# Kernel tuning notes

Hardware: AMD Instinct MI355X
Metric: run time of the kernel (lower is better)

The kernel has to match this reference:

```python
import math
import jax, jax.numpy as jnp
import numpy as np

B, L, D, H = 2, 2048, 1024, 16
DT = D // H  # 64


def setup_inputs() -> dict:
    key = jax.random.key(0)
    ks = jax.random.split(key, 11)
    s = 1.0 / math.sqrt(D)
    return {
        "q": jax.random.normal(ks[0], (B, L, D), jnp.float32),
        "k": jax.random.normal(ks[1], (B, L, D), jnp.float32),
        "v": jax.random.normal(ks[2], (B, L, D), jnp.float32),
        "Wq": jax.random.normal(ks[3], (D, D), jnp.float32) * s,
        "bq": jnp.zeros((D,), jnp.float32),
        "Wk": jax.random.normal(ks[4], (D, D), jnp.float32) * s,
        "bk": jnp.zeros((D,), jnp.float32),
        "Wv": jax.random.normal(ks[5], (D, D), jnp.float32) * s,
        "bv": jnp.zeros((D,), jnp.float32),
        "Wc": jax.random.normal(ks[6], (D, D), jnp.float32) * s,
        "bc": jnp.zeros((D,), jnp.float32),
    }


def reference(q, k, v, Wq, bq, Wk, bk, Wv, bv, Wc, bc):
    # Linear projections (torch Linear: x @ W^T + b)
    Q = q @ Wq.T + bq
    K = k @ Wk.T + bk
    V = v @ Wv.T + bv
    # split(): plain view/reshape [B, L, D] -> [B, H, L, d] (faithful to source)
    Qs = Q.reshape(B, H, L, DT)
    Ks = K.reshape(B, H, L, DT)
    Vs = V.reshape(B, H, L, DT)
    # k_t is also a plain reshape [B,H,L,d] -> [B,H,d,L] (NOT a transpose)
    Kt = Ks.reshape(B, H, DT, L)
    score = jnp.matmul(Qs, Kt) / math.sqrt(DT)  # [B, H, L, L]
    # nn.Softmax() with no dim on 4D tensor -> legacy dim=1 (head axis)
    attn = jax.nn.softmax(score, axis=1)
    out = jnp.matmul(attn, Vs)  # [B, H, L, d]
    out = out.reshape(B, L, D)  # concat() is also a plain reshape
    return out @ Wc.T + bc
```

## Files before the change

### kernel.cpp

```cpp
#include <hip/hip_runtime.h>
#include <hip/hip_bf16.h>


using u16   = unsigned short;
using f16   = _Float16;
using f16x2 = _Float16 __attribute__((ext_vector_type(2)));
using f16x8 = _Float16 __attribute__((ext_vector_type(8)));
using bf16x8 = __bf16 __attribute__((ext_vector_type(8)));
using f32x4  = float  __attribute__((ext_vector_type(4)));

__device__ __forceinline__ u16 f2bf(float f) {
    __bf16 h = (__bf16)f;
    return __builtin_bit_cast(u16, h);
}
__device__ __forceinline__ float ex2(float x) {
    return __builtin_amdgcn_exp2f(x);
}
__device__ __forceinline__ bf16x8 ldfrag(const u16* p) {
    bf16x8 r; __builtin_memcpy(&r, p, 16); return r;
}
__device__ __forceinline__ f16x8 ldfrag16(const u16* p) {
    f16x8 r; __builtin_memcpy(&r, p, 16); return r;
}
__device__ __forceinline__ unsigned pkrtz(float a, float b) {
    return __builtin_bit_cast(unsigned, __builtin_amdgcn_cvt_pkrtz(a, b));
}
__device__ __forceinline__ f16x2 u2h(unsigned u) { return __builtin_bit_cast(f16x2, u); }
__device__ __forceinline__ unsigned h2u(f16x2 h) { return __builtin_bit_cast(unsigned, h); }

__device__ __forceinline__ void stage16(const float* p, u16* d) {
    #pragma unroll
    for (int u = 0; u < 16; u += 4) {
        float4 t = *reinterpret_cast<const float4*>(p + u);
        d[u + 0] = f2bf(t.x); d[u + 1] = f2bf(t.y);
        d[u + 2] = f2bf(t.z); d[u + 3] = f2bf(t.w);
    }
}
__device__ __forceinline__ void stage16(const u16* p, u16* d) {
    #pragma unroll
    for (int u = 0; u < 16; u += 8)
        *reinterpret_cast<uint4*>(d + u) = *reinterpret_cast<const uint4*>(p + u);
}

template <typename XT, typename WT, typename OT, bool F16O>
__device__ __forceinline__ void gemm_body(
    const XT* __restrict__ X,
    const WT* __restrict__ W, const float* __restrict__ bias,
    OT* __restrict__ C, float scale,
    u16 (*lX)[72], u16 (*lW)[72])
{
    const int tid  = threadIdx.x;
    const int lane = tid & 63;
    const int wv   = tid >> 6;
    const int wm   = (wv >> 2) * 64;
    const int wn   = (wv & 3) * 32;
    const int m0 = blockIdx.x * 128;
    const int n0 = blockIdx.y * 128;
    const int sr = tid >> 2;
    const int sq = (tid & 3) * 16;
    const int fm = lane & 15;
    const int g  = lane >> 4;
    const int fk = g * 8;

    f32x4 acc[4][2] = {};

    for (int k0 = 0; k0 < 1024; k0 += 64) {
        stage16(X + (size_t)(m0 + sr) * 1024 + k0 + sq, &lX[sr][sq]);
        stage16(W + (size_t)(n0 + sr) * 1024 + k0 + sq, &lW[sr][sq]);
        __syncthreads();
        #pragma unroll
        for (int kb = 0; kb < 2; ++kb) {
            bf16x8 a[4], bb[2];
            #pragma unroll
            for (int mb = 0; mb < 4; ++mb)
                a[mb] = ldfrag(&lX[wm + mb * 16 + fm][kb * 32 + fk]);
            #pragma unroll
            for (int nb = 0; nb < 2; ++nb)
                bb[nb] = ldfrag(&lW[wn + nb * 16 + fm][kb * 32 + fk]);
            #pragma unroll
            for (int mb = 0; mb < 4; ++mb)
                #pragma unroll
                for (int nb = 0; nb < 2; ++nb)
                    acc[mb][nb] = __builtin_amdgcn_mfma_f32_16x16x32_bf16(
                        a[mb], bb[nb], acc[mb][nb], 0, 0, 0);
        }
        __syncthreads();
    }

    #pragma unroll
    for (int mb = 0; mb < 4; ++mb) {
        #pragma unroll
        for (int nb = 0; nb < 2; ++nb) {
            const int row = m0 + wm + mb * 16 + g * 4;
            const int col = n0 + wn + nb * 16 + fm;
            const float bv = bias[col];
            #pragma unroll
            for (int r = 0; r < 4; ++r) {
                const float val = (acc[mb][nb][r] + bv) * scale;
                OT* p = C + (size_t)(row + r) * 1024 + col;
                if constexpr (F16O) {
                    f16 h = (f16)val;
                    *p = __builtin_bit_cast(u16, h);
                } else if constexpr (__is_same(OT, u16)) {
                    *p = f2bf(val);
                } else {
                    *p = val;
                }
            }
        }
    }
}

template <typename T>
__global__ __launch_bounds__(512) void gemm_qkv_t(
    const T* __restrict__ q, const T* __restrict__ k,
    const T* __restrict__ v,
    const T* __restrict__ Wq, const float* __restrict__ bq,
    const T* __restrict__ Wk, const float* __restrict__ bk,
    const T* __restrict__ Wv, const float* __restrict__ bv,
    u16* __restrict__ Q16, u16* __restrict__ K16, u16* __restrict__ V16,
    float qscale)
{
    __shared__ u16 lX[128][72];
    __shared__ u16 lW[128][72];
    const int z = blockIdx.z;
    const T* X = (z == 0) ? q  : (z == 1) ? k  : v;
    const T* W = (z == 0) ? Wq : (z == 1) ? Wk : Wv;
    const float* B = (z == 0) ? bq : (z == 1) ? bk : bv;
    u16*         C = (z == 0) ? Q16 : (z == 1) ? K16 : V16;
    const float  s = (z == 0) ? qscale : 1.0f;
    gemm_body<T, T, u16, true>(X, W, B, C, s, lX, lW);
}

template <typename WT>
__global__ __launch_bounds__(512) void gemm_final_t(
    const u16* __restrict__ X,
    const WT* __restrict__ W, const float* __restrict__ bias,
    float* __restrict__ C)
{
    __shared__ u16 lX[128][72];
    __shared__ u16 lW[128][72];
    gemm_body<u16, WT, float, false>(X, W, bias, C, 1.0f, lX, lW);
}

__global__ __launch_bounds__(256) void prep_bf16(
    const float* __restrict__ q, const float* __restrict__ k,
    const float* __restrict__ v,
    const float* __restrict__ Wq, const float* __restrict__ Wk,
    const float* __restrict__ Wv, const float* __restrict__ Wc,
    u16* __restrict__ qb, u16* __restrict__ kb, u16* __restrict__ vb,
    u16* __restrict__ wqb, u16* __restrict__ wkb,
    u16* __restrict__ wvb, u16* __restrict__ wcb)
{
    const long long NC = 2097152;
    for (long long c = (long long)blockIdx.x * 256 + threadIdx.x; c < NC;
         c += (long long)gridDim.x * 256) {
        const float* src; u16* dst; long long off;
        if (c < 1572864) {
            if (c < 524288)       { src = q; dst = qb; off = c; }
            else if (c < 1048576) { src = k; dst = kb; off = c - 524288; }
            else                  { src = v; dst = vb; off = c - 1048576; }
        } else {
            const long long wI = c - 1572864;
            if (wI < 131072)      { src = Wq; dst = wqb; off = wI; }
            else if (wI < 262144) { src = Wk; dst = wkb; off = wI - 131072; }
            else if (wI < 393216) { src = Wv; dst = wvb; off = wI - 262144; }
            else                  { src = Wc; dst = wcb; off = wI - 393216; }
        }
        const float* p = src + off * 8;
        const float4 a  = reinterpret_cast<const float4*>(p)[0];
        const float4 b2 = reinterpret_cast<const float4*>(p)[1];
        u16 d[8];
        d[0] = f2bf(a.x);  d[1] = f2bf(a.y);  d[2] = f2bf(a.z);  d[3] = f2bf(a.w);
        d[4] = f2bf(b2.x); d[5] = f2bf(b2.y); d[6] = f2bf(b2.z); d[7] = f2bf(b2.w);
        *reinterpret_cast<uint4*>(dst + off * 8) = *reinterpret_cast<uint4*>(d);
    }
}

template <int NS>
__global__ __launch_bounds__(256) void presum_o(
    const u16* __restrict__ a, const u16* __restrict__ b,
    const u16* __restrict__ c, const u16* __restrict__ d,
    u16* __restrict__ o)
{
    const long long NC = 524288;
    for (long long i = (long long)blockIdx.x * 256 + threadIdx.x; i < NC;
         i += (long long)gridDim.x * 256) {
        const long long e0 = i * 8;
        const bf16x8 va = ldfrag(a + e0);
        const bf16x8 vb = ldfrag(b + e0);
        bf16x8 vc, vd;
        if constexpr (NS >= 3) vc = ldfrag(c + e0);
        if constexpr (NS >= 4) vd = ldfrag(d + e0);
        u16 r[8];
        #pragma unroll
        for (int e = 0; e < 8; ++e) {
            float s = (float)va[e] + (float)vb[e];
            if constexpr (NS >= 3) s += (float)vc[e];
            if constexpr (NS >= 4) s += (float)vd[e];
            r[e] = f2bf(s);
        }
        *reinterpret_cast<uint4*>(o + e0) = *reinterpret_cast<uint4*>(r);
    }
}

__global__ __launch_bounds__(256) void tp_kv2(
    const u16* __restrict__ kin, u16* __restrict__ kout,
    const u16* __restrict__ vin, u16* __restrict__ vout)
{
    __shared__ u16 t[64][80];
    const int which = (blockIdx.x >> 10) & 1;
    const int bx    = blockIdx.x & 1023;
    const u16* in_  = which ? vin  : kin;
    u16*       out_ = which ? vout : kout;
    const int tid = threadIdx.x;
    const int bh  = bx >> 5;
    const int tt  = bx & 31;
    const size_t base = (size_t)bh * 131072;
    const int C         = which ? 64 : 2048;
    const int r0        = which ? tt * 64 : 0;
    const int c0        = which ? 0 : tt * 64;
    const int outstride = which ? 2048 : 64;
    const u16* in = in_ + base;
    u16* out      = out_ + base;

    #pragma unroll
    for (int half = 0; half < 2; ++half) {
        const int rr = (tid >> 3) + half * 32;
        const int cb = tid & 7;
        const int cbs = cb ^ ((rr >> 3) & 7);
        *reinterpret_cast<uint4*>(&t[rr][cbs * 8]) =
            *reinterpret_cast<const uint4*>(in + (size_t)(r0 + rr) * C + c0 + cb * 8);
    }
    __syncthreads();
    #pragma unroll
    for (int half = 0; half < 2; ++half) {
        const int c  = (tid >> 3) + half * 32;
        const int rb = tid & 7;
        u16 vv[8];
        #pragma unroll
        for (int e = 0; e < 8; ++e) {
            const int r = rb * 8 + e;
            const int cbs2 = (c >> 3) ^ ((r >> 3) & 7);
            vv[e] = t[r][cbs2 * 8 + (c & 7)];
        }
        *reinterpret_cast<uint4*>(out + (size_t)(c0 + c) * outstride + r0 + rb * 8) =
            *reinterpret_cast<uint4*>(vv);
    }
}

__global__ __launch_bounds__(1024) void attn_fused(
    const u16* __restrict__ Qb, const u16* __restrict__ KT,
    const u16* __restrict__ VT, u16* __restrict__ O0,
    u16* __restrict__ O1, u16* __restrict__ O2, u16* __restrict__ O3,
    int jsplit)
{
    __shared__ unsigned expS[16][64][20];
    __shared__ unsigned rcpS[64][20];

    const int tid  = threadIdx.x;
    const int w    = tid >> 6;
    const int lane = tid & 63;
    const int fm   = lane & 15;
    const int g    = lane >> 4;
    const int fk   = g * 8;
    const int g4   = g * 4;
    const int g2   = g * 2;

    int b, it, js;
    u16* Ob;
    if (jsplit == 4) {
        const int grp = blockIdx.x & 7;
        b  = grp >> 2;
        js = grp & 3;
        it = blockIdx.x >> 3;
        Ob = (js == 0) ? O0 : (js == 1) ? O1 : (js == 2) ? O2 : O3;
    } else if (jsplit == 2) {
        const int grp = blockIdx.x & 3;
        b  = grp >> 1;
        js = grp & 1;
        it = blockIdx.x >> 2;
        Ob = js ? O1 : O0;
    } else {
        b  = blockIdx.x >> 5;
        it = blockIdx.x & 31;
        js = 0;
        Ob = O0;
    }
    const int jlen  = 2048 / jsplit;
    const int jbase = js * jlen;
    const int i0    = it * 64;
    const size_t hb = ((size_t)b * 2048 + (size_t)w * 128) * 1024;

    f16x8 qa[4][2];
    #pragma unroll
    for (int m = 0; m < 4; ++m)
        #pragma unroll
        for (int kb = 0; kb < 2; ++kb)
            qa[m][kb] = ldfrag16(Qb + hb + (size_t)(i0 + m * 16 + fm) * 64 + kb * 32 + fk);

    f32x4 oacc[4][4] = {};

    const int nt  = jlen >> 5;

    auto qk_tile = [&](int j0) {
        f16x8 kf[2][2];
        #pragma unroll
        for (int kb = 0; kb < 2; ++kb)
            #pragma unroll
            for (int nb = 0; nb < 2; ++nb)
                kf[kb][nb] = ldfrag16(KT + hb + (size_t)(j0 + nb * 16 + fm) * 64
                                               + kb * 32 + fk);
        #pragma unroll
        for (int m = 0; m < 4; ++m) {
            f32x4 st[2] = {};
            #pragma unroll
            for (int kb = 0; kb < 2; ++kb)
                #pragma unroll
                for (int nb = 0; nb < 2; ++nb)
                    st[nb] = __builtin_amdgcn_mfma_f32_16x16x32_f16(
                        kf[kb][nb], qa[m][kb], st[nb], 0, 0, 0);
            const int row = m * 16 + fm;
            #pragma unroll
            for (int nb = 0; nb < 2; ++nb) {
                uint2 ew2;
                ew2.x = pkrtz(ex2(st[nb][0]), ex2(st[nb][1]));
                ew2.y = pkrtz(ex2(st[nb][2]), ex2(st[nb][3]));
                *reinterpret_cast<uint2*>(&expS[w][row][nb * 8 + g2]) = ew2;
            }
        }
    };

    qk_tile(jbase);

    for (int t = 0; t < nt; ++t) {
        const int j0 = jbase + (t << 5);
        __syncthreads();
        f16x8 vf[4];
        #pragma unroll
        for (int nb = 0; nb < 4; ++nb)
            vf[nb] = ldfrag16(VT + hb + (size_t)(nb * 16 + fm) * 2048 + j0 + fk);
        {
            const int i  = tid >> 4;
            const int jp = tid & 15;
            unsigned eh[16];
            #pragma unroll
            for (int h = 0; h < 16; ++h) eh[h] = expS[h][i][jp];
            const f16x2 s0 = (u2h(eh[0])  + u2h(eh[1]))  + (u2h(eh[2])  + u2h(eh[3]));
            const f16x2 s1 = (u2h(eh[4])  + u2h(eh[5]))  + (u2h(eh[6])  + u2h(eh[7]));
            const f16x2 s2 = (u2h(eh[8])  + u2h(eh[9]))  + (u2h(eh[10]) + u2h(eh[11]));
            const f16x2 s3 = (u2h(eh[12]) + u2h(eh[13])) + (u2h(eh[14]) + u2h(eh[15]));
            const f16x2 ts = (s0 + s1) + (s2 + s3);
            rcpS[i][jp] = pkrtz(__builtin_amdgcn_rcpf((float)ts[0]),
                                __builtin_amdgcn_rcpf((float)ts[1]));
        }
        __syncthreads();
        #pragma unroll
        for (int m = 0; m < 4; ++m) {
            const int row = m * 16 + fm;
            const uint4 ew = *reinterpret_cast<const uint4*>(&expS[w][row][g4]);
            const uint4 rw = *reinterpret_cast<const uint4*>(&rcpS[row][g4]);
            uint4 pw;
            pw.x = h2u(u2h(ew.x) * u2h(rw.x));
            pw.y = h2u(u2h(ew.y) * u2h(rw.y));
            pw.z = h2u(u2h(ew.z) * u2h(rw.z));
            pw.w = h2u(u2h(ew.w) * u2h(rw.w));
            const f16x8 pa = __builtin_bit_cast(f16x8, pw);
            #pragma unroll
            for (int nb = 0; nb < 4; ++nb)
                oacc[m][nb] = __builtin_amdgcn_mfma_f32_16x16x32_f16(
                    pa, vf[nb], oacc[m][nb], 0, 0, 0);
        }
        if (t + 1 < nt) qk_tile(j0 + 32);
    }

    #pragma unroll
    for (int m = 0; m < 4; ++m)
        #pragma unroll
        for (int nb = 0; nb < 4; ++nb)
            #pragma unroll
            for (int r = 0; r < 4; ++r) {
                const int i = i0 + m * 16 + g4 + r;
                Ob[hb + (size_t)i * 64 + nb * 16 + fm] = f2bf(oacc[m][nb][r]);
            }
}

extern "C" void kernel_launch(void* const* d_in, const int* in_sizes, int n_in,
                              void* d_out, int out_size, void* d_ws, size_t ws_size,
                              hipStream_t stream)
{
    const float* q  = (const float*)d_in[0];
    const float* k  = (const float*)d_in[1];
    const float* v  = (const float*)d_in[2];
    const float* Wq = (const float*)d_in[3];
    const float* bq = (const float*)d_in[4];
    const float* Wk = (const float*)d_in[5];
    const float* bk = (const float*)d_in[6];
    const float* Wv = (const float*)d_in[7];
    const float* bv = (const float*)d_in[8];
    const float* Wc = (const float*)d_in[9];
    const float* bc = (const float*)d_in[10];
    float* out = (float*)d_out;

    const size_t MD = (size_t)4096 * 1024;
    const size_t WM = MD / 4;
    u16* W0 = (u16*)d_ws;
    u16* W1 = W0 + MD;
    u16* W2 = W1 + MD;
    u16* W3 = W2 + MD;
    u16* W4 = W3 + MD;
    u16* W5 = W4 + MD;
    u16* W6 = W5 + MD;
    u16* qb  = W6 + MD;
    u16* kb  = qb + MD;
    u16* vb  = kb + MD;
    u16* wqb = vb + MD;
    u16* wkb = wqb + WM;
    u16* wvb = wkb + WM;
    u16* wcb = wvb + WM;

    int jsplit = 1;
    if      (ws_size >= 7 * MD * sizeof(u16)) jsplit = 4;
    else if (ws_size >= 5 * MD * sizeof(u16)) jsplit = 2;
    const bool prep = ws_size >= 11 * MD * sizeof(u16);

    const float qscale = 0.125f * 1.4426950408889634f;

    if (prep)
        prep_bf16<<<dim3(2048), dim3(256), 0, stream>>>(
            q, k, v, Wq, Wk, Wv, Wc, qb, kb, vb, wqb, wkb, wvb, wcb);

    if (prep)
        gemm_qkv_t<u16><<<dim3(32, 8, 3), dim3(512), 0, stream>>>(
            qb, kb, vb, wqb, bq, wkb, bk, wvb, bv, W0, W1, W2, qscale);
    else
        gemm_qkv_t<float><<<dim3(32, 8, 3), dim3(512), 0, stream>>>(
            q, k, v, Wq, bq, Wk, bk, Wv, bv, W0, W1, W2, qscale);

    tp_kv2<<<dim3(2048), dim3(256), 0, stream>>>(W1, W3, W2, W4);

    const int agrid = (jsplit == 4) ? 256 : (jsplit == 2) ? 128 : 64;
    attn_fused<<<dim3(agrid), dim3(1024), 0, stream>>>(
        W0, W3, W4, W1, W2, W5, W6, jsplit);

    const u16* Xf = W1;
    if (jsplit == 4) {
        presum_o<4><<<dim3(2048), dim3(256), 0, stream>>>(W1, W2, W5, W6, W0);
        Xf = W0;
    } else if (jsplit == 2) {
        presum_o<2><<<dim3(2048), dim3(256), 0, stream>>>(W1, W2, nullptr, nullptr, W0);
        Xf = W0;
    }

    if (prep)
        gemm_final_t<u16><<<dim3(32, 8), dim3(512), 0, stream>>>(Xf, wcb, bc, out);
    else
        gemm_final_t<float><<<dim3(32, 8), dim3(512), 0, stream>>>(Xf, Wc, bc, out);
}
```

Measured before the change: 184.2 us.

## Retile fused attention to 512-thread blocks handling two heads per wave

Each attention block now covers 32 query rows instead of 64 and uses 512 threads. Each wave processes two heads rather than one. The grid doubles, the shared exp and reciprocal buffers halve, and launch bounds request four blocks per CU, all aimed at higher occupancy and cheaper block-wide barriers. In exchange, each K and V fragment load is reused across only 32 query rows, so K/V traffic from L2 per unit of work doubles.

```diff
diff --git a/kernel.cpp b/kernel.cpp
--- a/kernel.cpp
+++ b/kernel.cpp
@@ -249,17 +249,18 @@
     }
 }
 
-__global__ __launch_bounds__(1024) void attn_fused(
+__global__ __launch_bounds__(512, 4) void attn_fused(
     const u16* __restrict__ Qb, const u16* __restrict__ KT,
     const u16* __restrict__ VT, u16* __restrict__ O0,
     u16* __restrict__ O1, u16* __restrict__ O2, u16* __restrict__ O3,
     int jsplit)
 {
-    __shared__ unsigned expS[16][64][20];
-    __shared__ unsigned rcpS[64][20];
+    __shared__ unsigned expS[16][32][20];
+    __shared__ unsigned rcpS[32][20];
 
     const int tid  = threadIdx.x;
-    const int w    = tid >> 6;
+    const int wv   = tid >> 6;
+    const int h0   = wv * 2;
     const int lane = tid & 63;
     const int fm   = lane & 15;
     const int g    = lane >> 4;
@@ -282,51 +283,59 @@
         it = blockIdx.x >> 2;
         Ob = js ? O1 : O0;
     } else {
-        b  = blockIdx.x >> 5;
-        it = blockIdx.x & 31;
+        b  = blockIdx.x & 1;
+        it = blockIdx.x >> 1;
         js = 0;
         Ob = O0;
     }
     const int jlen  = 2048 / jsplit;
     const int jbase = js * jlen;
-    const int i0    = it * 64;
-    const size_t hb = ((size_t)b * 2048 + (size_t)w * 128) * 1024;
-
-    f16x8 qa[4][2];
-    #pragma unroll
-    for (int m = 0; m < 4; ++m)
-        #pragma unroll
-        for (int kb = 0; kb < 2; ++kb)
-            qa[m][kb] = ldfrag16(Qb + hb + (size_t)(i0 + m * 16 + fm) * 64 + kb * 32 + fk);
-
-    f32x4 oacc[4][4] = {};
+    const int i0    = it * 32;
+    size_t hb[2];
+    hb[0] = ((size_t)b * 2048 + (size_t)h0 * 128) * 1024;
+    hb[1] = hb[0] + 131072;
+
+    f16x8 qa[2][2][2];
+    #pragma unroll
+    for (int hh = 0; hh < 2; ++hh)
+        #pragma unroll
+        for (int m = 0; m < 2; ++m)
+            #pragma unroll
+            for (int kb = 0; kb < 2; ++kb)
+                qa[hh][m][kb] = ldfrag16(Qb + hb[hh]
+                    + (size_t)(i0 + m * 16 + fm) * 64 + kb * 32 + fk);
+
+    f32x4 oacc[2][2][4] = {};
 
     const int nt  = jlen >> 5;
 
     auto qk_tile = [&](int j0) {
-        f16x8 kf[2][2];
-        #pragma unroll
-        for (int kb = 0; kb < 2; ++kb)
-            #pragma unroll
-            for (int nb = 0; nb < 2; ++nb)
-                kf[kb][nb] = ldfrag16(KT + hb + (size_t)(j0 + nb * 16 + fm) * 64
-                                               + kb * 32 + fk);
-        #pragma unroll
-        for (int m = 0; m < 4; ++m) {
-            f32x4 st[2] = {};
+        #pragma unroll
+        for (int hh = 0; hh < 2; ++hh) {
+            f16x8 kf[2][2];
             #pragma unroll
             for (int kb = 0; kb < 2; ++kb)
                 #pragma unroll
                 for (int nb = 0; nb < 2; ++nb)
-                    st[nb] = __builtin_amdgcn_mfma_f32_16x16x32_f16(
-                        kf[kb][nb], qa[m][kb], st[nb], 0, 0, 0);
-            const int row = m * 16 + fm;
-            #pragma unroll
-            for (int nb = 0; nb < 2; ++nb) {
-                uint2 ew2;
-                ew2.x = pkrtz(ex2(st[nb][0]), ex2(st[nb][1]));
-                ew2.y = pkrtz(ex2(st[nb][2]), ex2(st[nb][3]));
-                *reinterpret_cast<uint2*>(&expS[w][row][nb * 8 + g2]) = ew2;
+                    kf[kb][nb] = ldfrag16(KT + hb[hh]
+                        + (size_t)(j0 + nb * 16 + fm) * 64 + kb * 32 + fk);
+            #pragma unroll
+            for (int m = 0; m < 2; ++m) {
+                f32x4 st[2] = {};
+                #pragma unroll
+                for (int kb = 0; kb < 2; ++kb)
+                    #pragma unroll
+                    for (int nb = 0; nb < 2; ++nb)
+                        st[nb] = __builtin_amdgcn_mfma_f32_16x16x32_f16(
+                            kf[kb][nb], qa[hh][m][kb], st[nb], 0, 0, 0);
+                const int row = m * 16 + fm;
+                #pragma unroll
+                for (int nb = 0; nb < 2; ++nb) {
+                    uint2 ew2;
+                    ew2.x = pkrtz(ex2(st[nb][0]), ex2(st[nb][1]));
+                    ew2.y = pkrtz(ex2(st[nb][2]), ex2(st[nb][3]));
+                    *reinterpret_cast<uint2*>(&expS[h0 + hh][row][nb * 8 + g2]) = ew2;
+                }
             }
         }
     };
@@ -336,10 +345,6 @@
     for (int t = 0; t < nt; ++t) {
         const int j0 = jbase + (t << 5);
         __syncthreads();
-        f16x8 vf[4];
-        #pragma unroll
-        for (int nb = 0; nb < 4; ++nb)
-            vf[nb] = ldfrag16(VT + hb + (size_t)(nb * 16 + fm) * 2048 + j0 + fk);
         {
             const int i  = tid >> 4;
             const int jp = tid & 15;
@@ -356,33 +361,44 @@
         }
         __syncthreads();
         #pragma unroll
-        for (int m = 0; m < 4; ++m) {
-            const int row = m * 16 + fm;
-            const uint4 ew = *reinterpret_cast<const uint4*>(&expS[w][row][g4]);
-            const uint4 rw = *reinterpret_cast<const uint4*>(&rcpS[row][g4]);
-            uint4 pw;
-            pw.x = h2u(u2h(ew.x) * u2h(rw.x));
-            pw.y = h2u(u2h(ew.y) * u2h(rw.y));
-            pw.z = h2u(u2h(ew.z) * u2h(rw.z));
-            pw.w = h2u(u2h(ew.w) * u2h(rw.w));
-            const f16x8 pa = __builtin_bit_cast(f16x8, pw);
+        for (int hh = 0; hh < 2; ++hh) {
+            f16x8 vf[4];
             #pragma unroll
             for (int nb = 0; nb < 4; ++nb)
-                oacc[m][nb] = __builtin_amdgcn_mfma_f32_16x16x32_f16(
-                    pa, vf[nb], oacc[m][nb], 0, 0, 0);
+                vf[nb] = ldfrag16(VT + hb[hh]
+                    + (size_t)(nb * 16 + fm) * 2048 + j0 + fk);
+            #pragma unroll
+            for (int m = 0; m < 2; ++m) {
+                const int row = m * 16 + fm;
+                const uint4 ew = *reinterpret_cast<const uint4*>(&expS[h0 + hh][row][g4]);
+                const uint4 rw = *reinterpret_cast<const uint4*>(&rcpS[row][g4]);
+                uint4 pw;
+                pw.x = h2u(u2h(ew.x) * u2h(rw.x));
+                pw.y = h2u(u2h(ew.y) * u2h(rw.y));
+                pw.z = h2u(u2h(ew.z) * u2h(rw.z));
+                pw.w = h2u(u2h(ew.w) * u2h(rw.w));
+                const f16x8 pa = __builtin_bit_cast(f16x8, pw);
+                #pragma unroll
+                for (int nb = 0; nb < 4; ++nb)
+                    oacc[hh][m][nb] = __builtin_amdgcn_mfma_f32_16x16x32_f16(
+                        pa, vf[nb], oacc[hh][m][nb], 0, 0, 0);
+            }
         }
         if (t + 1 < nt) qk_tile(j0 + 32);
     }
 
     #pragma unroll
-    for (int m = 0; m < 4; ++m)
-        #pragma unroll
-        for (int nb = 0; nb < 4; ++nb)
-            #pragma unroll
-            for (int r = 0; r < 4; ++r) {
-                const int i = i0 + m * 16 + g4 + r;
-                Ob[hb + (size_t)i * 64 + nb * 16 + fm] = f2bf(oacc[m][nb][r]);
-            }
+    for (int hh = 0; hh < 2; ++hh)
+        #pragma unroll
+        for (int m = 0; m < 2; ++m)
+            #pragma unroll
+            for (int nb = 0; nb < 4; ++nb)
+                #pragma unroll
+                for (int r = 0; r < 4; ++r) {
+                    const int i = i0 + m * 16 + g4 + r;
+                    Ob[hb[hh] + (size_t)i * 64 + nb * 16 + fm] =
+                        f2bf(oacc[hh][m][nb][r]);
+                }
 }
 
 extern "C" void kernel_launch(void* const* d_in, const int* in_sizes, int n_in,
@@ -439,8 +455,8 @@
 
     tp_kv2<<<dim3(2048), dim3(256), 0, stream>>>(W1, W3, W2, W4);
 
-    const int agrid = (jsplit == 4) ? 256 : (jsplit == 2) ? 128 : 64;
-    attn_fused<<<dim3(agrid), dim3(1024), 0, stream>>>(
+    const int agrid = (jsplit == 4) ? 512 : (jsplit == 2) ? 256 : 128;
+    attn_fused<<<dim3(agrid), dim3(512), 0, stream>>>(
         W0, W3, W4, W1, W2, W5, W6, jsplit);
 
     const u16* Xf = W1;
```

Measured after the change: 257.2 us. 39.6% more time.

## Process 64-column tiles per barrier pair with XOR-swizzled shared exp buffers

Applied to the files above, without the earlier changes.

Doubles the key-column tile handled per iteration of the head-axis softmax attention loop from 32 to 64, so each pair of block-wide barriers covers twice as much work. This halves the number of __syncthreads calls. The shared exp and reciprocal buffers are widened to 32 columns and indexed with an XOR swizzle to avoid LDS bank conflicts, since the old padding-based layout no longer applies. It uses more shared memory and more live work per stage, which may reduce latency hiding.

```diff
diff --git a/kernel.cpp b/kernel.cpp
--- a/kernel.cpp
+++ b/kernel.cpp
@@ -255,8 +255,8 @@
     u16* __restrict__ O1, u16* __restrict__ O2, u16* __restrict__ O3,
     int jsplit)
 {
-    __shared__ unsigned expS[16][64][20];
-    __shared__ unsigned rcpS[64][20];
+    __shared__ unsigned expS[16][64][32];
+    __shared__ unsigned rcpS[64][32];
 
     const int tid  = threadIdx.x;
     const int w    = tid >> 6;
@@ -292,6 +292,8 @@
     const int i0    = it * 64;
     const size_t hb = ((size_t)b * 2048 + (size_t)w * 128) * 1024;
 
+    auto fx = [](int r) { return ((r >> 1) & 3) << 2; };
+
     f16x8 qa[4][2];
     #pragma unroll
     for (int m = 0; m < 4; ++m)
@@ -301,9 +303,9 @@
 
     f32x4 oacc[4][4] = {};
 
-    const int nt  = jlen >> 5;
-
-    auto qk_tile = [&](int j0) {
+    const int nt = jlen >> 6;
+
+    auto qk_half = [&](int j0, int cb) {
         f16x8 kf[2][2];
         #pragma unroll
         for (int kb = 0; kb < 2; ++kb)
@@ -321,45 +323,28 @@
                     st[nb] = __builtin_amdgcn_mfma_f32_16x16x32_f16(
                         kf[kb][nb], qa[m][kb], st[nb], 0, 0, 0);
             const int row = m * 16 + fm;
+            const int fr  = fx(row);
             #pragma unroll
             for (int nb = 0; nb < 2; ++nb) {
                 uint2 ew2;
                 ew2.x = pkrtz(ex2(st[nb][0]), ex2(st[nb][1]));
                 ew2.y = pkrtz(ex2(st[nb][2]), ex2(st[nb][3]));
-                *reinterpret_cast<uint2*>(&expS[w][row][nb * 8 + g2]) = ew2;
+                *reinterpret_cast<uint2*>(&expS[w][row][(cb + nb * 8 + g2) ^ fr]) = ew2;
             }
         }
     };
 
-    qk_tile(jbase);
-
-    for (int t = 0; t < nt; ++t) {
-        const int j0 = jbase + (t << 5);
-        __syncthreads();
+    auto pv_half = [&](int jh, int cb) {
         f16x8 vf[4];
         #pragma unroll
         for (int nb = 0; nb < 4; ++nb)
-            vf[nb] = ldfrag16(VT + hb + (size_t)(nb * 16 + fm) * 2048 + j0 + fk);
-        {
-            const int i  = tid >> 4;
-            const int jp = tid & 15;
-            unsigned eh[16];
-            #pragma unroll
-            for (int h = 0; h < 16; ++h) eh[h] = expS[h][i][jp];
-            const f16x2 s0 = (u2h(eh[0])  + u2h(eh[1]))  + (u2h(eh[2])  + u2h(eh[3]));
-            const f16x2 s1 = (u2h(eh[4])  + u2h(eh[5]))  + (u2h(eh[6])  + u2h(eh[7]));
-            const f16x2 s2 = (u2h(eh[8])  + u2h(eh[9]))  + (u2h(eh[10]) + u2h(eh[11]));
-            const f16x2 s3 = (u2h(eh[12]) + u2h(eh[13])) + (u2h(eh[14]) + u2h(eh[15]));
-            const f16x2 ts = (s0 + s1) + (s2 + s3);
-            rcpS[i][jp] = pkrtz(__builtin_amdgcn_rcpf((float)ts[0]),
-                                __builtin_amdgcn_rcpf((float)ts[1]));
-        }
-        __syncthreads();
+            vf[nb] = ldfrag16(VT + hb + (size_t)(nb * 16 + fm) * 2048 + jh + fk);
         #pragma unroll
         for (int m = 0; m < 4; ++m) {
             const int row = m * 16 + fm;
-            const uint4 ew = *reinterpret_cast<const uint4*>(&expS[w][row][g4]);
-            const uint4 rw = *reinterpret_cast<const uint4*>(&rcpS[row][g4]);
+            const int fr  = fx(row);
+            const uint4 ew = *reinterpret_cast<const uint4*>(&expS[w][row][(cb + g4) ^ fr]);
+            const uint4 rw = *reinterpret_cast<const uint4*>(&rcpS[row][(cb + g4) ^ fr]);
             uint4 pw;
             pw.x = h2u(u2h(ew.x) * u2h(rw.x));
             pw.y = h2u(u2h(ew.y) * u2h(rw.y));
@@ -371,7 +356,41 @@
                 oacc[m][nb] = __builtin_amdgcn_mfma_f32_16x16x32_f16(
                     pa, vf[nb], oacc[m][nb], 0, 0, 0);
         }
-        if (t + 1 < nt) qk_tile(j0 + 32);
+    };
+
+    auto sum_half = [&](int i, int p) {
+        unsigned eh[16];
+        #pragma unroll
+        for (int h = 0; h < 16; ++h) eh[h] = expS[h][i][p];
+        const f16x2 s0 = (u2h(eh[0])  + u2h(eh[1]))  + (u2h(eh[2])  + u2h(eh[3]));
+        const f16x2 s1 = (u2h(eh[4])  + u2h(eh[5]))  + (u2h(eh[6])  + u2h(eh[7]));
+        const f16x2 s2 = (u2h(eh[8])  + u2h(eh[9]))  + (u2h(eh[10]) + u2h(eh[11]));
+        const f16x2 s3 = (u2h(eh[12]) + u2h(eh[13])) + (u2h(eh[14]) + u2h(eh[15]));
+        const f16x2 ts = (s0 + s1) + (s2 + s3);
+        rcpS[i][p] = pkrtz(__builtin_amdgcn_rcpf((float)ts[0]),
+                           __builtin_amdgcn_rcpf((float)ts[1]));
+    };
+
+    qk_half(jbase, 0);
+    qk_half(jbase + 32, 16);
+
+    for (int t = 0; t < nt; ++t) {
+        const int j0 = jbase + (t << 6);
+        __syncthreads();
+        {
+            const int i = tid >> 4;
+            const int p = (tid & 15) ^ fx(i);
+            sum_half(i, p);
+            __builtin_amdgcn_sched_barrier(0);
+            sum_half(i, p + 16);
+        }
+        __syncthreads();
+        pv_half(j0, 0);
+        pv_half(j0 + 32, 16);
+        if (t + 1 < nt) {
+            qk_half(j0 + 64, 0);
+            qk_half(j0 + 96, 16);
+        }
     }
 
     #pragma unroll
```

Measured after the change: 231.3 us. 1.26x slower.

## Fuse K transpose into K projection GEMM epilogue via LDS staging

Applied to the files above, without the earlier changes.

The K projection moves into its own GEMM kernel whose epilogue stages the tile in shared memory and writes it directly in the transposed per-head layout the attention kernel expects. This removes the K half of the separate transpose kernel, cutting one global write and read of K. The QKV GEMM becomes a Q/V-only launch and the transpose kernel now handles only V. This adds an extra kernel launch and a less coalesced transposed store path. The float-input variant stages via stage16, which looks type-dependent and may not handle float inputs correctly.

```diff
diff --git a/kernel.cpp b/kernel.cpp
--- a/kernel.cpp
+++ b/kernel.cpp
@@ -112,24 +112,102 @@
 }
 
 template <typename T>
-__global__ __launch_bounds__(512) void gemm_qkv_t(
-    const T* __restrict__ q, const T* __restrict__ k,
-    const T* __restrict__ v,
+__global__ __launch_bounds__(512) void gemm_qv_t(
+    const T* __restrict__ q, const T* __restrict__ v,
     const T* __restrict__ Wq, const float* __restrict__ bq,
-    const T* __restrict__ Wk, const float* __restrict__ bk,
     const T* __restrict__ Wv, const float* __restrict__ bv,
-    u16* __restrict__ Q16, u16* __restrict__ K16, u16* __restrict__ V16,
-    float qscale)
+    u16* __restrict__ Q16, u16* __restrict__ V16, float qscale)
 {
     __shared__ u16 lX[128][72];
     __shared__ u16 lW[128][72];
     const int z = blockIdx.z;
-    const T* X = (z == 0) ? q  : (z == 1) ? k  : v;
-    const T* W = (z == 0) ? Wq : (z == 1) ? Wk : Wv;
-    const float* B = (z == 0) ? bq : (z == 1) ? bk : bv;
-    u16*         C = (z == 0) ? Q16 : (z == 1) ? K16 : V16;
-    const float  s = (z == 0) ? qscale : 1.0f;
+    const T* X = z ? v  : q;
+    const T* W = z ? Wv : Wq;
+    const float* B = z ? bv : bq;
+    u16*         C = z ? V16 : Q16;
+    const float  s = z ? 1.0f : qscale;
     gemm_body<T, T, u16, true>(X, W, B, C, s, lX, lW);
+}
+
+template <typename T>
+__global__ __launch_bounds__(512) void gemm_kt_t(
+    const T* __restrict__ X, const T* __restrict__ W,
+    const float* __restrict__ bias, u16* __restrict__ KT)
+{
+    __shared__ u16 lbuf[2][128][72];
+    u16 (*lX)[72] = lbuf[0];
+    u16 (*lW)[72] = lbuf[1];
+
+    const int tid  = threadIdx.x;
+    const int lane = tid & 63;
+    const int wv   = tid >> 6;
+    const int wm   = (wv >> 2) * 64;
+    const int wn   = (wv & 3) * 32;
+    const int m0 = blockIdx.x * 128;
+    const int n0 = blockIdx.y * 128;
+    const int sr = tid >> 2;
+    const int sq = (tid & 3) * 16;
+    const int fm = lane & 15;
+    const int g  = lane >> 4;
+    const int fk = g * 8;
+
+    f32x4 acc[4][2] = {};
+
+    for (int k0 = 0; k0 < 1024; k0 += 64) {
+        stage16(X + (size_t)(m0 + sr) * 1024 + k0 + sq, &lX[sr][sq]);
+        stage16(W + (size_t)(n0 + sr) * 1024 + k0 + sq, &lW[sr][sq]);
+        __syncthreads();
+        #pragma unroll
+        for (int kb = 0; kb < 2; ++kb) {
+            bf16x8 a[4], bb[2];
+            #pragma unroll
+            for (int mb = 0; mb < 4; ++mb)
+                a[mb] = ldfrag(&lX[wm + mb * 16 + fm][kb * 32 + fk]);
+            #pragma unroll
+            for (int nb = 0; nb < 2; ++nb)
+                bb[nb] = ldfrag(&lW[wn + nb * 16 + fm][kb * 32 + fk]);
+            #pragma unroll
+            for (int mb = 0; mb < 4; ++mb)
+                #pragma unroll
+                for (int nb = 0; nb < 2; ++nb)
+                    acc[mb][nb] = __builtin_amdgcn_mfma_f32_16x16x32_bf16(
+                        a[mb], bb[nb], acc[mb][nb], 0, 0, 0);
+        }
+        __syncthreads();
+    }
+
+    u16 (*T2)[136] = reinterpret_cast<u16 (*)[136]>(&lbuf[0][0][0]);
+    #pragma unroll
+    for (int mb = 0; mb < 4; ++mb)
+        #pragma unroll
+        for (int nb = 0; nb < 2; ++nb) {
+            const int colL = wn + nb * 16 + fm;
+            const float bv = bias[n0 + colL];
+            #pragma unroll
+            for (int r = 0; r < 4; ++r) {
+                const int row = wm + mb * 16 + g * 4 + r;
+                const f16 hv = (f16)(acc[mb][nb][r] + bv);
+                T2[row][colL] = __builtin_bit_cast(u16, hv);
+            }
+        }
+    __syncthreads();
+
+    const int bb2 = m0 >> 11;
+    const int hh  = (m0 >> 7) & 15;
+    u16* slab = KT + (size_t)bb2 * 2097152 + (size_t)hh * 131072;
+    const int kr   = tid >> 1;
+    const int half = tid & 1;
+    const int hi   = kr >> 7;
+    const int jloc = kr & 127;
+    u16 buf[32];
+    #pragma unroll
+    for (int e = 0; e < 32; ++e)
+        buf[e] = T2[64 * half + 2 * e + hi][jloc];
+    u16* dst = slab + (size_t)((hi << 10) + n0 + jloc) * 64 + half * 32;
+    #pragma unroll
+    for (int q2 = 0; q2 < 4; ++q2)
+        *reinterpret_cast<uint4*>(dst + q2 * 8) =
+            *reinterpret_cast<const uint4*>(buf + q2 * 8);
 }
 
 template <typename WT>
@@ -204,25 +282,18 @@
     }
 }
 
-__global__ __launch_bounds__(256) void tp_kv2(
-    const u16* __restrict__ kin, u16* __restrict__ kout,
+__global__ __launch_bounds__(256) void tp_v(
     const u16* __restrict__ vin, u16* __restrict__ vout)
 {
     __shared__ u16 t[64][80];
-    const int which = (blockIdx.x >> 10) & 1;
-    const int bx    = blockIdx.x & 1023;
-    const u16* in_  = which ? vin  : kin;
-    u16*       out_ = which ? vout : kout;
+    const int bx = blockIdx.x;
     const int tid = threadIdx.x;
     const int bh  = bx >> 5;
     const int tt  = bx & 31;
     const size_t base = (size_t)bh * 131072;
-    const int C         = which ? 64 : 2048;
-    const int r0        = which ? tt * 64 : 0;
-    const int c0        = which ? 0 : tt * 64;
-    const int outstride = which ? 2048 : 64;
-    const u16* in = in_ + base;
-    u16* out      = out_ + base;
+    const int r0 = tt * 64;
+    const u16* in = vin + base;
+    u16* out      = vout + base;
 
     #pragma unroll
     for (int half = 0; half < 2; ++half) {
@@ -230,7 +301,7 @@
         const int cb = tid & 7;
         const int cbs = cb ^ ((rr >> 3) & 7);
         *reinterpret_cast<uint4*>(&t[rr][cbs * 8]) =
-            *reinterpret_cast<const uint4*>(in + (size_t)(r0 + rr) * C + c0 + cb * 8);
+            *reinterpret_cast<const uint4*>(in + (size_t)(r0 + rr) * 64 + cb * 8);
     }
     __syncthreads();
     #pragma unroll
@@ -244,7 +315,7 @@
             const int cbs2 = (c >> 3) ^ ((r >> 3) & 7);
             vv[e] = t[r][cbs2 * 8 + (c & 7)];
         }
-        *reinterpret_cast<uint4*>(out + (size_t)(c0 + c) * outstride + r0 + rb * 8) =
+        *reinterpret_cast<uint4*>(out + (size_t)c * 2048 + r0 + rb * 8) =
             *reinterpret_cast<uint4*>(vv);
     }
 }
@@ -430,14 +501,17 @@
         prep_bf16<<<dim3(2048), dim3(256), 0, stream>>>(
             q, k, v, Wq, Wk, Wv, Wc, qb, kb, vb, wqb, wkb, wvb, wcb);
 
-    if (prep)
-        gemm_qkv_t<u16><<<dim3(32, 8, 3), dim3(512), 0, stream>>>(
-            qb, kb, vb, wqb, bq, wkb, bk, wvb, bv, W0, W1, W2, qscale);
-    else
-        gemm_qkv_t<float><<<dim3(32, 8, 3), dim3(512), 0, stream>>>(
-            q, k, v, Wq, bq, Wk, bk, Wv, bv, W0, W1, W2, qscale);
-
-    tp_kv2<<<dim3(2048), dim3(256), 0, stream>>>(W1, W3, W2, W4);
+    if (prep) {
+        gemm_qv_t<u16><<<dim3(32, 8, 2), dim3(512), 0, stream>>>(
+            qb, vb, wqb, bq, wvb, bv, W0, W2, qscale);
+        gemm_kt_t<u16><<<dim3(32, 8), dim3(512), 0, stream>>>(kb, wkb, bk, W3);
+    } else {
+        gemm_qv_t<float><<<dim3(32, 8, 2), dim3(512), 0, stream>>>(
+            q, v, Wq, bq, Wv, bv, W0, W2, qscale);
+        gemm_kt_t<float><<<dim3(32, 8), dim3(512), 0, stream>>>(k, Wk, bk, W3);
+    }
+
+    tp_v<<<dim3(1024), dim3(256), 0, stream>>>(W2, W4);
 
     const int agrid = (jsplit == 4) ? 256 : (jsplit == 2) ? 128 : 64;
     attn_fused<<<dim3(agrid), dim3(1024), 0, stream>>>(
```

Result: slower. 195.8 us (+6.3%).
